# Kernel optimization log

Hardware: AMD Instinct MI355X
Metric: run time of the kernel (lower is better)

The kernel has to match this reference:

```python
import jax, jax.numpy as jnp
import numpy as np

DIM, H, DH = 3072, 24, 128
MLP = int(DIM * 4.0)
EPS = 1e-6


def setup_inputs() -> dict:
    key = jax.random.key(0)
    ks = jax.random.split(key, 8)
    B, L = 2, 4096
    s = 0.02
    return {
        "hidden_states": jax.random.normal(ks[0], (B, L, DIM), jnp.float32),
        "temb": jax.random.normal(ks[1], (B, DIM), jnp.float32),
        "rope": jax.random.normal(ks[2], (L, DH // 2, 4), jnp.float32),
        "w_lin": jax.random.normal(ks[3], (DIM, 3 * DIM), jnp.float32) * s,
        "b_lin": jnp.zeros((3 * DIM,), jnp.float32),
        "w1": jax.random.normal(ks[4], (DIM, 3 * DIM + MLP), jnp.float32) * s,
        "b1": jnp.zeros((3 * DIM + MLP,), jnp.float32),
        "w2": jax.random.normal(ks[5], (DIM + MLP, DIM), jnp.float32) * s,
        "b2": jnp.zeros((DIM,), jnp.float32),
        "q_scale": jnp.ones((DH,), jnp.float32),
        "k_scale": jnp.ones((DH,), jnp.float32),
    }


def _rms(x, scale):
    return x * jax.lax.rsqrt(jnp.mean(x * x, axis=-1, keepdims=True) + EPS) * scale


def _rope(x, fr):
    # x: [B,H,L,DH]; fr: [L, DH//2, 2, 2]
    B, Hn, L, D = x.shape
    x_ = x.reshape(B, Hn, L, D // 2, 1, 2)
    out = fr[..., 0] * x_[..., 0] + fr[..., 1] * x_[..., 1]  # [B,H,L,D//2,2]
    return out.reshape(B, Hn, L, D)


def reference(hidden_states, temb, rope, w_lin, b_lin, w1, b1, w2, b2, q_scale, k_scale):
    B, L, _ = hidden_states.shape
    residual = hidden_states
    # AdaLayerNormZeroSingle
    emb = jax.nn.silu(temb) @ w_lin + b_lin  # [B, 3*DIM]
    shift, scale, gate = jnp.split(emb[:, None, :], 3, axis=-1)
    mu = jnp.mean(hidden_states, axis=-1, keepdims=True)
    var = jnp.mean(jnp.square(hidden_states - mu), axis=-1, keepdims=True)
    x = (hidden_states - mu) * jax.lax.rsqrt(var + EPS)
    x = x * (1 + scale) + shift
    # fused QKV + MLP projection
    proj = x @ w1 + b1
    qkv, mlp = proj[..., : 3 * DIM], proj[..., 3 * DIM :]
    qkv = qkv.reshape(B, L, 3, H, DH).transpose(2, 0, 3, 1, 4)  # [3,B,H,L,DH]
    q, k, v = qkv[0], qkv[1], qkv[2]
    q = _rms(q, q_scale)
    k = _rms(k, k_scale)
    fr = rope.reshape(L, DH // 2, 2, 2)
    q = _rope(q, fr)
    k = _rope(k, fr)
    # heads are MERGED before attention (faithful to source)
    q = q.transpose(0, 2, 1, 3).reshape(B, L, H * DH)
    k = k.transpose(0, 2, 1, 3).reshape(B, L, H * DH)
    v = v.transpose(0, 2, 1, 3).reshape(B, L, H * DH)
    attn = jax.nn.softmax(jnp.einsum("bqd,bkd->bqk", q, k) * (DH ** -0.5), axis=-1)
    attn_out = jnp.einsum("bqk,bkd->bqd", attn, v)
    h = jnp.concatenate([attn_out, jax.nn.gelu(mlp)], axis=-1) @ w2 + b2
    return residual + gate * h
```

## Files before the change

kernel.cpp:

```cpp
#include <hip/hip_runtime.h>
#include <hip/hip_fp16.h>

typedef _Float16 half_t;
typedef __attribute__((ext_vector_type(8))) _Float16 f16x8;
typedef __attribute__((ext_vector_type(4))) float f32x4;

#define DIM   3072
#define NH    24
#define DH    128
#define MLP_D 12288
#define LSEQ  4096
#define BATCH 2
#define NROWS 8192
#define N1    21504
#define QKV_N 9216
#define CAT_N 15360

__device__ __forceinline__ void gload16(const void* g, void* l) {
  __builtin_amdgcn_global_load_lds((const __attribute__((address_space(1))) void*)g,
                                   (__attribute__((address_space(3))) void*)l, 16, 0, 0);
}

__device__ __forceinline__ float gelu_tanh(float x) {
  float u = 0.7978845608028654f * (x + 0.044715f * x * x * x);
  float t = 1.f - 2.f / (__expf(2.f * u) + 1.f);
  return 0.5f * x * (1.f + t);
}

struct EpiParams {
  const float* bias;
  float* outF; int ldoF;
  half_t* o1; int ldo1;
  half_t* o2; int ldo2;
  const float* resid;
  const float* gate;
  float scale;
};

template<int EPI>
__global__ __launch_bounds__(512, 2) void gemm256(
    const half_t* __restrict__ A, int lda,
    const half_t* __restrict__ B, int ldb,
    int nbx, int nby, int nsplit, int K, EpiParams ep)
{
  __shared__ __align__(16) char lds[131072];
  const int t = threadIdx.x, lane = t & 63, wid = t >> 6;

  const int nwg = nbx * nby;
  const int wg = blockIdx.x;
  const int id = (wg & 7) * (nwg >> 3) + (wg >> 3);
  const int panel = 8 * nbx;
  const int bm = (id / panel) * 8 + (id % 8);
  const int bn = (id % panel) / 8;
  const int brow = bm * 256, bcol = bn * 256;
  const int wr = wid >> 2, wc = wid & 3;

  f32x4 acc[8][4];
#pragma unroll
  for (int m = 0; m < 8; ++m)
#pragma unroll
    for (int n = 0; n < 4; ++n) acc[m][n] = (f32x4){0.f, 0.f, 0.f, 0.f};

  const int sperm = (((lane & 7) ^ (lane >> 3)) * 8);
  const half_t* pA = A + (size_t)(brow + wid * 32 + (lane >> 3)) * lda + sperm;
  const half_t* pB = B + (size_t)(bcol + wid * 32 + (lane >> 3)) * ldb + sperm;
  char* ldsA = lds + wid * 4096;
  const int NT = K >> 6;

#define STAGE(bufsel, tk)                                                  \
  {                                                                        \
    char* la = ldsA + (bufsel) * 65536;                                    \
    const half_t* ga = pA + (size_t)(tk) * 64;                             \
    const half_t* gb = pB + (size_t)(tk) * 64;                             \
    _Pragma("unroll")                                                      \
    for (int c = 0; c < 4; ++c) {                                          \
      gload16(ga + (size_t)c * 8 * lda, la + c * 1024);                    \
      gload16(gb + (size_t)c * 8 * ldb, la + 32768 + c * 1024);            \
    }                                                                      \
  }

  STAGE(0, 0);
  STAGE(1, 1);

  const int laneR = lane & 15;
  const int slot0 = (((lane >> 4) ^ (lane & 7)) << 4);
  const char* arow0 = lds + (size_t)(wr * 128 + laneR) * 128;
  const char* brow0 = lds + 32768 + (size_t)(wc * 64 + laneR) * 128;

  for (int tt = 0; tt < NT; ++tt) {
    const int cur = tt & 1;
    if (tt == NT - 1) asm volatile("s_waitcnt vmcnt(0)" ::: "memory");
    else              asm volatile("s_waitcnt vmcnt(8)" ::: "memory");
    __builtin_amdgcn_s_barrier();
    __builtin_amdgcn_sched_barrier(0);

    const char* ar = arow0 + cur * 65536;
    const char* br = brow0 + cur * 65536;
#pragma unroll
    for (int kk = 0; kk < 2; ++kk) {
      const int slot = slot0 ^ (kk << 6);
      f16x8 af[8], bf[4];
#pragma unroll
      for (int mi = 0; mi < 8; ++mi) af[mi] = *(const f16x8*)(ar + mi * 2048 + slot);
#pragma unroll
      for (int nj = 0; nj < 4; ++nj) bf[nj] = *(const f16x8*)(br + nj * 2048 + slot);
#pragma unroll
      for (int mi = 0; mi < 8; ++mi)
#pragma unroll
        for (int nj = 0; nj < 4; ++nj)
          acc[mi][nj] = __builtin_amdgcn_mfma_f32_16x16x32_f16(af[mi], bf[nj], acc[mi][nj], 0, 0, 0);
    }

    asm volatile("" ::: "memory");
    __builtin_amdgcn_sched_barrier(0);
    __builtin_amdgcn_s_barrier();
    if (tt + 2 < NT) STAGE(cur, tt + 2);
  }
#undef STAGE

  const int colb = bcol + wc * 64;
  const int rowb = brow + wr * 128 + (lane >> 4) * 4;
#pragma unroll
  for (int mi = 0; mi < 8; ++mi) {
#pragma unroll
    for (int nj = 0; nj < 4; ++nj) {
      int col = colb + nj * 16 + laneR;
#pragma unroll
      for (int j = 0; j < 4; ++j) {
        int row = rowb + mi * 16 + j;
        float v = acc[mi][nj][j];
        if (EPI == 0) {
          v += ep.bias[col];
          if (col < nsplit) {
            ep.o1[(size_t)row * ep.ldo1 + col] = (half_t)v;
          } else {
            ep.o2[(size_t)row * ep.ldo2 + DIM + (col - nsplit)] = (half_t)gelu_tanh(v);
          }
        } else if (EPI == 1) {
          ep.outF[(size_t)row * ep.ldoF + col] = v * ep.scale;
        } else if (EPI == 2) {
          ep.o2[(size_t)row * ep.ldo2 + col] = (half_t)v;
        } else {
          v += ep.bias[col];
          int b = row >> 12;
          float g = ep.gate[(size_t)b * QKV_N + col];
          float r = ep.resid[(size_t)row * DIM + col];
          ep.outF[(size_t)row * ep.ldoF + col] = r + g * v;
        }
      }
    }
  }
}

__global__ __launch_bounds__(256) void k_emb(
    const float* __restrict__ temb, const float* __restrict__ w_lin,
    const float* __restrict__ b_lin, float* __restrict__ emb)
{
  __shared__ float s[DIM];
  int b = blockIdx.y;
  int col = blockIdx.x * 256 + threadIdx.x;
  const float* tr = temb + (size_t)b * DIM;
  for (int k = threadIdx.x; k < DIM; k += 256) {
    float x = tr[k];
    s[k] = x / (1.f + __expf(-x));
  }
  __syncthreads();
  float acc = b_lin[col];
  for (int k = 0; k < DIM; k += 4) {
    acc += s[k] * w_lin[(size_t)k * QKV_N + col]
         + s[k + 1] * w_lin[(size_t)(k + 1) * QKV_N + col]
         + s[k + 2] * w_lin[(size_t)(k + 2) * QKV_N + col]
         + s[k + 3] * w_lin[(size_t)(k + 3) * QKV_N + col];
  }
  emb[(size_t)b * QKV_N + col] = acc;
}

__global__ __launch_bounds__(256) void k_lnmod(
    const float* __restrict__ hs, const float* __restrict__ emb,
    half_t* __restrict__ xmod)
{
  int row = blockIdx.x;
  int b = row >> 12;
  const float* x = hs + (size_t)row * DIM;
  int t = threadIdx.x;
  float s = 0.f, s2 = 0.f;
  float4 v[3];
#pragma unroll
  for (int i = 0; i < 3; ++i) {
    v[i] = ((const float4*)x)[t + 256 * i];
    s  += v[i].x + v[i].y + v[i].z + v[i].w;
    s2 += v[i].x * v[i].x + v[i].y * v[i].y + v[i].z * v[i].z + v[i].w * v[i].w;
  }
  for (int o = 32; o; o >>= 1) { s += __shfl_xor(s, o); s2 += __shfl_xor(s2, o); }
  __shared__ float rs[4], rs2[4];
  int lane = t & 63, w = t >> 6;
  if (lane == 0) { rs[w] = s; rs2[w] = s2; }
  __syncthreads();
  s = rs[0] + rs[1] + rs[2] + rs[3];
  s2 = rs2[0] + rs2[1] + rs2[2] + rs2[3];
  float mu = s * (1.f / DIM);
  float var = s2 * (1.f / DIM) - mu * mu;
  float rstd = rsqrtf(var + 1e-6f);
  const float* shift = emb + (size_t)b * QKV_N;
  const float* scale = shift + DIM;
#pragma unroll
  for (int i = 0; i < 3; ++i) {
    int g = t + 256 * i;
    float4 sc = ((const float4*)scale)[g];
    float4 sh = ((const float4*)shift)[g];
    half_t ob[4];
    float vv[4] = {v[i].x, v[i].y, v[i].z, v[i].w};
    float scv[4] = {sc.x, sc.y, sc.z, sc.w};
    float shv[4] = {sh.x, sh.y, sh.z, sh.w};
#pragma unroll
    for (int j = 0; j < 4; ++j) {
      float xn = (vv[j] - mu) * rstd;
      ob[j] = (half_t)(xn * (1.f + scv[j]) + shv[j]);
    }
    *(uint2*)&xmod[(size_t)row * DIM + g * 4] = *(uint2*)ob;
  }
}

__global__ __launch_bounds__(256) void k_transpose_cvt(
    const float* __restrict__ in, half_t* __restrict__ out, int R, int C)
{
  __shared__ float s[64][65];
  int c0 = blockIdx.x * 64, r0 = blockIdx.y * 64;
  int tx = threadIdx.x & 63, ty = threadIdx.x >> 6;
#pragma unroll
  for (int j = 0; j < 16; ++j) {
    int r = ty + j * 4;
    s[r][tx] = in[(size_t)(r0 + r) * C + c0 + tx];
  }
  __syncthreads();
#pragma unroll
  for (int j = 0; j < 16; ++j) {
    int c = ty + j * 4;
    out[(size_t)(c0 + c) * R + r0 + tx] = (half_t)s[tx][c];
  }
}

__global__ __launch_bounds__(256) void k_qk_rmsrope(
    half_t* __restrict__ qkv, const float* __restrict__ rope,
    const float* __restrict__ q_scale, const float* __restrict__ k_scale)
{
  int w = blockIdx.x * 4 + (threadIdx.x >> 6);
  int lane = threadIdx.x & 63;
  int qk = w & 1;
  int hr = w >> 1;
  int h = hr % 24;
  int bl = hr / 24;
  size_t base = (size_t)bl * QKV_N + qk * DIM + h * DH;
  float x0 = (float)qkv[base + lane * 2];
  float x1 = (float)qkv[base + lane * 2 + 1];
  float ss = x0 * x0 + x1 * x1;
  for (int o = 32; o; o >>= 1) ss += __shfl_xor(ss, o);
  float r = rsqrtf(ss * (1.f / DH) + 1e-6f);
  const float* sc = qk ? k_scale : q_scale;
  float xs0 = x0 * r * sc[lane * 2];
  float xs1 = x1 * r * sc[lane * 2 + 1];
  int l = bl & (LSEQ - 1);
  float4 fr = ((const float4*)rope)[(size_t)l * 64 + lane];
  qkv[base + lane * 2]     = (half_t)(fr.x * xs0 + fr.y * xs1);
  qkv[base + lane * 2 + 1] = (half_t)(fr.z * xs0 + fr.w * xs1);
}

__global__ __launch_bounds__(256) void k_vT(
    const half_t* __restrict__ qkv, half_t* __restrict__ vT)
{
  __shared__ half_t s[64][65];
  int b = blockIdx.z;
  int l0 = blockIdx.x * 64, d0 = blockIdx.y * 64;
  int tx = threadIdx.x & 63, ty = threadIdx.x >> 6;
#pragma unroll
  for (int j = 0; j < 16; ++j) {
    int l = ty + j * 4;
    s[l][tx] = qkv[(size_t)(b * LSEQ + l0 + l) * QKV_N + 2 * DIM + d0 + tx];
  }
  __syncthreads();
#pragma unroll
  for (int j = 0; j < 16; ++j) {
    int d = ty + j * 4;
    vT[((size_t)b * DIM + d0 + d) * LSEQ + l0 + tx] = s[tx][d];
  }
}

__global__ __launch_bounds__(256) void k_softmax(
    const float* __restrict__ S, half_t* __restrict__ P)
{
  int row = blockIdx.x;
  const float* srow = S + (size_t)row * LSEQ;
  int t = threadIdx.x;
  float4 v[4];
  float mx = -1e30f;
#pragma unroll
  for (int i = 0; i < 4; ++i) {
    v[i] = ((const float4*)srow)[t + 256 * i];
    mx = fmaxf(mx, fmaxf(fmaxf(v[i].x, v[i].y), fmaxf(v[i].z, v[i].w)));
  }
  for (int o = 32; o; o >>= 1) mx = fmaxf(mx, __shfl_xor(mx, o));
  __shared__ float rmx[4], rsum[4];
  int lane = t & 63, w = t >> 6;
  if (lane == 0) rmx[w] = mx;
  __syncthreads();
  mx = fmaxf(fmaxf(rmx[0], rmx[1]), fmaxf(rmx[2], rmx[3]));
  float s = 0.f;
#pragma unroll
  for (int i = 0; i < 4; ++i) {
    v[i].x = __expf(v[i].x - mx); v[i].y = __expf(v[i].y - mx);
    v[i].z = __expf(v[i].z - mx); v[i].w = __expf(v[i].w - mx);
    s += v[i].x + v[i].y + v[i].z + v[i].w;
  }
  for (int o = 32; o; o >>= 1) s += __shfl_xor(s, o);
  if (lane == 0) rsum[w] = s;
  __syncthreads();
  s = rsum[0] + rsum[1] + rsum[2] + rsum[3];
  float inv = 1.f / s;
#pragma unroll
  for (int i = 0; i < 4; ++i) {
    half_t ob[4] = {
      (half_t)(v[i].x * inv), (half_t)(v[i].y * inv),
      (half_t)(v[i].z * inv), (half_t)(v[i].w * inv)};
    *(uint2*)&P[(size_t)row * LSEQ + (t + 256 * i) * 4] = *(uint2*)ob;
  }
}

extern "C" void kernel_launch(void* const* d_in, const int* in_sizes, int n_in,
                              void* d_out, int out_size, void* d_ws, size_t ws_size,
                              hipStream_t stream) {
  const float* hs      = (const float*)d_in[0];
  const float* temb    = (const float*)d_in[1];
  const float* rope    = (const float*)d_in[2];
  const float* w_lin   = (const float*)d_in[3];
  const float* b_lin   = (const float*)d_in[4];
  const float* w1      = (const float*)d_in[5];
  const float* b1      = (const float*)d_in[6];
  const float* w2      = (const float*)d_in[7];
  const float* b2      = (const float*)d_in[8];
  const float* q_scale = (const float*)d_in[9];
  const float* k_scale = (const float*)d_in[10];
  float* out = (float*)d_out;

  char* ws = (char*)d_ws;
  size_t off = 0;
  auto alloc = [&](size_t bytes) { char* p = ws + off; off += (bytes + 255) & ~(size_t)255; return p; };
  float*  emb    = (float*) alloc((size_t)BATCH * QKV_N * 4);
  half_t* xmod   = (half_t*)alloc((size_t)NROWS * DIM * 2);
  half_t* w1T    = (half_t*)alloc((size_t)N1 * DIM * 2);
  half_t* w2T    = (half_t*)alloc((size_t)DIM * CAT_N * 2);
  half_t* qkv    = (half_t*)alloc((size_t)NROWS * QKV_N * 2);
  half_t* concat = (half_t*)alloc((size_t)NROWS * CAT_N * 2);
  half_t* vT     = (half_t*)alloc((size_t)BATCH * DIM * LSEQ * 2);
  float*  Sbuf   = (float*) alloc((size_t)LSEQ * LSEQ * 4);
  half_t* Pbuf   = (half_t*)alloc((size_t)LSEQ * LSEQ * 2);
  (void)ws_size; (void)n_in; (void)in_sizes; (void)out_size;

  k_emb<<<dim3(QKV_N / 256, BATCH), 256, 0, stream>>>(temb, w_lin, b_lin, emb);
  k_transpose_cvt<<<dim3(N1 / 64, DIM / 64), 256, 0, stream>>>(w1, w1T, DIM, N1);
  k_transpose_cvt<<<dim3(DIM / 64, CAT_N / 64), 256, 0, stream>>>(w2, w2T, CAT_N, DIM);
  k_lnmod<<<NROWS, 256, 0, stream>>>(hs, emb, xmod);

  EpiParams ep1 = {b1, nullptr, 0, qkv, QKV_N, concat, CAT_N, nullptr, nullptr, 0.f};
  gemm256<0><<<(N1 / 256) * (NROWS / 256), 512, 0, stream>>>(
      xmod, DIM, w1T, DIM, N1 / 256, NROWS / 256, QKV_N, DIM, ep1);

  k_qk_rmsrope<<<(NROWS * NH * 2) / 4, 256, 0, stream>>>(qkv, rope, q_scale, k_scale);
  k_vT<<<dim3(LSEQ / 64, DIM / 64, BATCH), 256, 0, stream>>>(qkv, vT);

  for (int b = 0; b < BATCH; ++b) {
    const half_t* qb = qkv + (size_t)b * LSEQ * QKV_N;
    EpiParams epS = {nullptr, Sbuf, LSEQ, nullptr, 0, nullptr, 0, nullptr, nullptr, 0.08838834764831845f};
    gemm256<1><<<(LSEQ / 256) * (LSEQ / 256), 512, 0, stream>>>(
        qb, QKV_N, qb + DIM, QKV_N, LSEQ / 256, LSEQ / 256, 0, DIM, epS);
    k_softmax<<<LSEQ, 256, 0, stream>>>(Sbuf, Pbuf);
    EpiParams epPV = {nullptr, nullptr, 0, nullptr, 0,
                      concat + (size_t)b * LSEQ * CAT_N, CAT_N, nullptr, nullptr, 0.f};
    gemm256<2><<<(DIM / 256) * (LSEQ / 256), 512, 0, stream>>>(
        Pbuf, LSEQ, vT + (size_t)b * DIM * LSEQ, LSEQ, DIM / 256, LSEQ / 256, 0, LSEQ, epPV);
  }

  EpiParams ep2 = {b2, out, DIM, nullptr, 0, nullptr, 0, hs, emb + 2 * DIM, 0.f};
  gemm256<3><<<(DIM / 256) * (NROWS / 256), 512, 0, stream>>>(
      concat, CAT_N, w2T, CAT_N, DIM / 256, NROWS / 256, 0, CAT_N, ep2);
}
```

Measured before the change: 3.053 ms.

## Split GEMM main loop into four interleaved phases with staggered async loads

```diff
diff --git a/kernel.cpp b/kernel.cpp
--- a/kernel.cpp
+++ b/kernel.cpp
@@ -61,63 +61,113 @@
 #pragma unroll
     for (int n = 0; n < 4; ++n) acc[m][n] = (f32x4){0.f, 0.f, 0.f, 0.f};
 
-  const int sperm = (((lane & 7) ^ (lane >> 3)) * 8);
-  const half_t* pA = A + (size_t)(brow + wid * 32 + (lane >> 3)) * lda + sperm;
-  const half_t* pB = B + (size_t)(bcol + wid * 32 + (lane >> 3)) * ldb + sperm;
-  char* ldsA = lds + wid * 4096;
+  const int scol = (((lane & 3) ^ ((lane >> 3) & 3)) * 8);
+  const half_t* pA = A + (size_t)(brow + wid * 32 + (lane >> 2)) * lda + scol;
+  const half_t* pB = B + (size_t)(bcol + wid * 32 + (lane >> 2)) * ldb + scol;
+  const int wrow = wid * 2048;
   const int NT = K >> 6;
 
-#define STAGE(bufsel, tk)                                                  \
-  {                                                                        \
-    char* la = ldsA + (bufsel) * 65536;                                    \
-    const half_t* ga = pA + (size_t)(tk) * 64;                             \
-    const half_t* gb = pB + (size_t)(tk) * 64;                             \
-    _Pragma("unroll")                                                      \
-    for (int c = 0; c < 4; ++c) {                                          \
-      gload16(ga + (size_t)c * 8 * lda, la + c * 1024);                    \
-      gload16(gb + (size_t)c * 8 * ldb, la + 32768 + c * 1024);            \
-    }                                                                      \
-  }
-
-  STAGE(0, 0);
-  STAGE(1, 1);
+  const int pc = (((lane >> 4) ^ ((lane >> 1) & 3)) << 4);
+  const int aoff = (wr * 128 + (lane & 15)) * 64 + pc;
+  const int boff = 32768 + (wc * 64 + (lane & 15)) * 64 + pc;
+
+  f16x8 bf[2][4];
+
+#define STAGE_A(bb, kh, tk) {                                               \
+    gload16(pA + (size_t)(tk) * 64 + (kh) * 32,                             \
+            (bb) + (kh) * 16384 + wrow);                                    \
+    gload16(pA + (size_t)(tk) * 64 + (kh) * 32 + (size_t)16 * lda,          \
+            (bb) + (kh) * 16384 + wrow + 1024); }
+#define STAGE_B(bb, kh, tk) {                                               \
+    gload16(pB + (size_t)(tk) * 64 + (kh) * 32,                             \
+            (bb) + 32768 + (kh) * 16384 + wrow);                            \
+    gload16(pB + (size_t)(tk) * 64 + (kh) * 32 + (size_t)16 * ldb,          \
+            (bb) + 32768 + (kh) * 16384 + wrow + 1024); }
+
+  {
+    char* b0 = lds;
+    char* b1 = lds + 65536;
+    STAGE_B(b0, 0, 0); STAGE_A(b0, 0, 0); STAGE_B(b0, 1, 0);
+    STAGE_A(b0, 1, 0); STAGE_B(b1, 0, 1); STAGE_A(b1, 0, 1); STAGE_B(b1, 1, 1);
+    asm volatile("s_waitcnt vmcnt(6)" ::: "memory");
+    __builtin_amdgcn_s_barrier();
+  }
+
+#define PHASE_TAIL                                                          \
+    __builtin_amdgcn_sched_barrier(0);                                      \
+    __builtin_amdgcn_s_barrier();                                           \
+    asm volatile("s_waitcnt lgkmcnt(0)" ::: "memory");                      \
+    __builtin_amdgcn_sched_barrier(0);                                      \
+    __builtin_amdgcn_s_setprio(1);
+
+#define PHASE_END                                                           \
+    __builtin_amdgcn_s_setprio(0);                                          \
+    __builtin_amdgcn_sched_barrier(0);                                      \
+    __builtin_amdgcn_s_barrier();
+
+  for (int tt = 0; tt < NT; ++tt) {
+    char* cb = lds + (size_t)(tt & 1) * 65536;
+    char* nb = lds + (size_t)((tt & 1) ^ 1) * 65536;
+    f16x8 af[4];
+
+#pragma unroll
+    for (int mi = 0; mi < 4; ++mi) af[mi] = *(const f16x8*)(cb + aoff + mi * 1024);
+#pragma unroll
+    for (int nj = 0; nj < 4; ++nj) bf[0][nj] = *(const f16x8*)(cb + boff + nj * 1024);
+    if (tt + 1 < NT) STAGE_A(nb, 1, tt + 1);
+    PHASE_TAIL
+#pragma unroll
+    for (int mi = 0; mi < 4; ++mi)
+#pragma unroll
+      for (int nj = 0; nj < 4; ++nj)
+        acc[mi][nj] = __builtin_amdgcn_mfma_f32_16x16x32_f16(af[mi], bf[0][nj], acc[mi][nj], 0, 0, 0);
+    PHASE_END
+
+#pragma unroll
+    for (int mi = 0; mi < 4; ++mi) af[mi] = *(const f16x8*)(cb + aoff + 4096 + mi * 1024);
+#pragma unroll
+    for (int nj = 0; nj < 4; ++nj) bf[1][nj] = *(const f16x8*)(cb + boff + 16384 + nj * 1024);
+    if (tt + 2 < NT) STAGE_B(cb, 0, tt + 2);
+    PHASE_TAIL
+#pragma unroll
+    for (int mi = 0; mi < 4; ++mi)
+#pragma unroll
+      for (int nj = 0; nj < 4; ++nj)
+        acc[4 + mi][nj] = __builtin_amdgcn_mfma_f32_16x16x32_f16(af[mi], bf[0][nj], acc[4 + mi][nj], 0, 0, 0);
+    PHASE_END
+
+#pragma unroll
+    for (int mi = 0; mi < 4; ++mi) af[mi] = *(const f16x8*)(cb + aoff + 16384 + mi * 1024);
+    if (tt + 2 < NT) STAGE_A(cb, 0, tt + 2);
+    PHASE_TAIL
+#pragma unroll
+    for (int mi = 0; mi < 4; ++mi)
+#pragma unroll
+      for (int nj = 0; nj < 4; ++nj)
+        acc[mi][nj] = __builtin_amdgcn_mfma_f32_16x16x32_f16(af[mi], bf[1][nj], acc[mi][nj], 0, 0, 0);
+    PHASE_END
+
+#pragma unroll
+    for (int mi = 0; mi < 4; ++mi) af[mi] = *(const f16x8*)(cb + aoff + 16384 + 4096 + mi * 1024);
+    if (tt + 2 < NT) STAGE_B(cb, 1, tt + 2);
+    PHASE_TAIL
+#pragma unroll
+    for (int mi = 0; mi < 4; ++mi)
+#pragma unroll
+      for (int nj = 0; nj < 4; ++nj)
+        acc[4 + mi][nj] = __builtin_amdgcn_mfma_f32_16x16x32_f16(af[mi], bf[1][nj], acc[4 + mi][nj], 0, 0, 0);
+    __builtin_amdgcn_s_setprio(0);
+    __builtin_amdgcn_sched_barrier(0);
+    if (tt + 2 < NT) asm volatile("s_waitcnt vmcnt(6)" ::: "memory");
+    else             asm volatile("s_waitcnt vmcnt(0)" ::: "memory");
+    __builtin_amdgcn_s_barrier();
+  }
+#undef STAGE_A
+#undef STAGE_B
+#undef PHASE_TAIL
+#undef PHASE_END
 
   const int laneR = lane & 15;
-  const int slot0 = (((lane >> 4) ^ (lane & 7)) << 4);
-  const char* arow0 = lds + (size_t)(wr * 128 + laneR) * 128;
-  const char* brow0 = lds + 32768 + (size_t)(wc * 64 + laneR) * 128;
-
-  for (int tt = 0; tt < NT; ++tt) {
-    const int cur = tt & 1;
-    if (tt == NT - 1) asm volatile("s_waitcnt vmcnt(0)" ::: "memory");
-    else              asm volatile("s_waitcnt vmcnt(8)" ::: "memory");
-    __builtin_amdgcn_s_barrier();
-    __builtin_amdgcn_sched_barrier(0);
-
-    const char* ar = arow0 + cur * 65536;
-    const char* br = brow0 + cur * 65536;
-#pragma unroll
-    for (int kk = 0; kk < 2; ++kk) {
-      const int slot = slot0 ^ (kk << 6);
-      f16x8 af[8], bf[4];
-#pragma unroll
-      for (int mi = 0; mi < 8; ++mi) af[mi] = *(const f16x8*)(ar + mi * 2048 + slot);
-#pragma unroll
-      for (int nj = 0; nj < 4; ++nj) bf[nj] = *(const f16x8*)(br + nj * 2048 + slot);
-#pragma unroll
-      for (int mi = 0; mi < 8; ++mi)
-#pragma unroll
-        for (int nj = 0; nj < 4; ++nj)
-          acc[mi][nj] = __builtin_amdgcn_mfma_f32_16x16x32_f16(af[mi], bf[nj], acc[mi][nj], 0, 0, 0);
-    }
-
-    asm volatile("" ::: "memory");
-    __builtin_amdgcn_sched_barrier(0);
-    __builtin_amdgcn_s_barrier();
-    if (tt + 2 < NT) STAGE(cur, tt + 2);
-  }
-#undef STAGE
-
   const int colb = bcol + wc * 64;
   const int rowb = brow + wr * 128 + (lane >> 4) * 4;
 #pragma unroll
```

New measurement: 2.930 ms. -4.0%, faster.

## Restructure GEMM main loop into 4-stage K=32 pipeline with register prefetch

Applied to the files above, without the earlier changes.

```diff
diff --git a/kernel.cpp b/kernel.cpp
--- a/kernel.cpp
+++ b/kernel.cpp
@@ -61,63 +61,87 @@
 #pragma unroll
     for (int n = 0; n < 4; ++n) acc[m][n] = (f32x4){0.f, 0.f, 0.f, 0.f};
 
-  const int sperm = (((lane & 7) ^ (lane >> 3)) * 8);
-  const half_t* pA = A + (size_t)(brow + wid * 32 + (lane >> 3)) * lda + sperm;
-  const half_t* pB = B + (size_t)(bcol + wid * 32 + (lane >> 3)) * ldb + sperm;
-  char* ldsA = lds + wid * 4096;
-  const int NT = K >> 6;
-
-#define STAGE(bufsel, tk)                                                  \
-  {                                                                        \
-    char* la = ldsA + (bufsel) * 65536;                                    \
-    const half_t* ga = pA + (size_t)(tk) * 64;                             \
-    const half_t* gb = pB + (size_t)(tk) * 64;                             \
-    _Pragma("unroll")                                                      \
-    for (int c = 0; c < 4; ++c) {                                          \
-      gload16(ga + (size_t)c * 8 * lda, la + c * 1024);                    \
-      gload16(gb + (size_t)c * 8 * ldb, la + 32768 + c * 1024);            \
-    }                                                                      \
-  }
-
-  STAGE(0, 0);
-  STAGE(1, 1);
+  const int scol = (((lane & 3) ^ ((lane >> 3) & 3)) * 8);
+  const half_t* pA = A + (size_t)(brow + wid * 32 + (lane >> 2)) * lda + scol;
+  const half_t* pB = B + (size_t)(bcol + wid * 32 + (lane >> 2)) * ldb + scol;
+  const int wrow = wid * 2048;
+  const int NT = K >> 5;
+
+  const int pc = (((lane >> 4) ^ ((lane >> 1) & 3)) << 4);
+  const int arow = (wr * 128 + (lane & 15)) * 64 + pc;
+  const int brow_o = 16384 + (wc * 64 + (lane & 15)) * 64 + pc;
+
+  f16x8 af[4], af2[4], bfA[4], bfB[4];
+
+#define STAGE(tk) {                                                         \
+    char* sb = lds + (((tk) & 3) << 15);                                    \
+    const half_t* ga = pA + (size_t)(tk) * 32;                              \
+    const half_t* gb = pB + (size_t)(tk) * 32;                              \
+    gload16(ga, sb + wrow);                                                 \
+    gload16(ga + (size_t)16 * lda, sb + wrow + 1024);                       \
+    gload16(gb, sb + 16384 + wrow);                                         \
+    gload16(gb + (size_t)16 * ldb, sb + 16384 + wrow + 1024); }
+
+#define MFMAC(base, AF, BF)                                                 \
+    __builtin_amdgcn_s_setprio(1);                                          \
+    _Pragma("unroll")                                                       \
+    for (int mi = 0; mi < 4; ++mi)                                          \
+      _Pragma("unroll")                                                     \
+      for (int nj = 0; nj < 4; ++nj)                                        \
+        acc[(base) + mi][nj] = __builtin_amdgcn_mfma_f32_16x16x32_f16(      \
+            AF[mi], BF[nj], acc[(base) + mi][nj], 0, 0, 0);                 \
+    __builtin_amdgcn_s_setprio(0);
+
+#define BODY(tt, BFC, BFN) {                                                \
+    char* cb = lds + (((tt) & 3) << 15);                                    \
+    af2[0] = *(const f16x8*)(cb + arow + 4096);                             \
+    af2[1] = *(const f16x8*)(cb + arow + 5120);                             \
+    af2[2] = *(const f16x8*)(cb + arow + 6144);                             \
+    af2[3] = *(const f16x8*)(cb + arow + 7168);                             \
+    MFMAC(0, af, BFC)                                                       \
+    if ((tt) + 3 < NT) STAGE((tt) + 3);                                     \
+    __builtin_amdgcn_sched_barrier(0);                                      \
+    if ((tt) + 3 < NT)      asm volatile("s_waitcnt vmcnt(8)" ::: "memory");\
+    else if ((tt) + 2 < NT) asm volatile("s_waitcnt vmcnt(4)" ::: "memory");\
+    else                    asm volatile("s_waitcnt vmcnt(0)" ::: "memory");\
+    __builtin_amdgcn_s_barrier();                                           \
+    __builtin_amdgcn_sched_barrier(0);                                      \
+    if ((tt) + 1 < NT) {                                                    \
+      char* fb = lds + ((((tt) + 1) & 3) << 15);                            \
+      af[0] = *(const f16x8*)(fb + arow);                                   \
+      af[1] = *(const f16x8*)(fb + arow + 1024);                            \
+      af[2] = *(const f16x8*)(fb + arow + 2048);                            \
+      af[3] = *(const f16x8*)(fb + arow + 3072);                            \
+      BFN[0] = *(const f16x8*)(fb + brow_o);                                \
+      BFN[1] = *(const f16x8*)(fb + brow_o + 1024);                         \
+      BFN[2] = *(const f16x8*)(fb + brow_o + 2048);                         \
+      BFN[3] = *(const f16x8*)(fb + brow_o + 3072);                         \
+    }                                                                       \
+    MFMAC(4, af2, BFC)                                                      \
+  }
+
+  STAGE(0); STAGE(1); STAGE(2);
+  asm volatile("s_waitcnt vmcnt(8)" ::: "memory");
+  __builtin_amdgcn_s_barrier();
+  __builtin_amdgcn_sched_barrier(0);
+  af[0] = *(const f16x8*)(lds + arow);
+  af[1] = *(const f16x8*)(lds + arow + 1024);
+  af[2] = *(const f16x8*)(lds + arow + 2048);
+  af[3] = *(const f16x8*)(lds + arow + 3072);
+  bfA[0] = *(const f16x8*)(lds + brow_o);
+  bfA[1] = *(const f16x8*)(lds + brow_o + 1024);
+  bfA[2] = *(const f16x8*)(lds + brow_o + 2048);
+  bfA[3] = *(const f16x8*)(lds + brow_o + 3072);
+
+  for (int tt = 0; tt < NT; tt += 2) {
+    BODY(tt, bfA, bfB)
+    BODY(tt + 1, bfB, bfA)
+  }
+#undef STAGE
+#undef MFMAC
+#undef BODY
 
   const int laneR = lane & 15;
-  const int slot0 = (((lane >> 4) ^ (lane & 7)) << 4);
-  const char* arow0 = lds + (size_t)(wr * 128 + laneR) * 128;
-  const char* brow0 = lds + 32768 + (size_t)(wc * 64 + laneR) * 128;
-
-  for (int tt = 0; tt < NT; ++tt) {
-    const int cur = tt & 1;
-    if (tt == NT - 1) asm volatile("s_waitcnt vmcnt(0)" ::: "memory");
-    else              asm volatile("s_waitcnt vmcnt(8)" ::: "memory");
-    __builtin_amdgcn_s_barrier();
-    __builtin_amdgcn_sched_barrier(0);
-
-    const char* ar = arow0 + cur * 65536;
-    const char* br = brow0 + cur * 65536;
-#pragma unroll
-    for (int kk = 0; kk < 2; ++kk) {
-      const int slot = slot0 ^ (kk << 6);
-      f16x8 af[8], bf[4];
-#pragma unroll
-      for (int mi = 0; mi < 8; ++mi) af[mi] = *(const f16x8*)(ar + mi * 2048 + slot);
-#pragma unroll
-      for (int nj = 0; nj < 4; ++nj) bf[nj] = *(const f16x8*)(br + nj * 2048 + slot);
-#pragma unroll
-      for (int mi = 0; mi < 8; ++mi)
-#pragma unroll
-        for (int nj = 0; nj < 4; ++nj)
-          acc[mi][nj] = __builtin_amdgcn_mfma_f32_16x16x32_f16(af[mi], bf[nj], acc[mi][nj], 0, 0, 0);
-    }
-
-    asm volatile("" ::: "memory");
-    __builtin_amdgcn_sched_barrier(0);
-    __builtin_amdgcn_s_barrier();
-    if (tt + 2 < NT) STAGE(cur, tt + 2);
-  }
-#undef STAGE
-
   const int colb = bcol + wc * 64;
   const int rowb = brow + wr * 128 + (lane >> 4) * 4;
 #pragma unroll
```

New measurement: 2.858 ms. 6.4% less time.

## Restructure GEMM mainloop into 4-stage BK=32 pipeline with split phases

Applied to the files above, without the earlier changes.

```diff
diff --git a/kernel.cpp b/kernel.cpp
--- a/kernel.cpp
+++ b/kernel.cpp
@@ -61,63 +61,87 @@
 #pragma unroll
     for (int n = 0; n < 4; ++n) acc[m][n] = (f32x4){0.f, 0.f, 0.f, 0.f};
 
-  const int sperm = (((lane & 7) ^ (lane >> 3)) * 8);
-  const half_t* pA = A + (size_t)(brow + wid * 32 + (lane >> 3)) * lda + sperm;
-  const half_t* pB = B + (size_t)(bcol + wid * 32 + (lane >> 3)) * ldb + sperm;
-  char* ldsA = lds + wid * 4096;
-  const int NT = K >> 6;
-
-#define STAGE(bufsel, tk)                                                  \
-  {                                                                        \
-    char* la = ldsA + (bufsel) * 65536;                                    \
-    const half_t* ga = pA + (size_t)(tk) * 64;                             \
-    const half_t* gb = pB + (size_t)(tk) * 64;                             \
-    _Pragma("unroll")                                                      \
-    for (int c = 0; c < 4; ++c) {                                          \
-      gload16(ga + (size_t)c * 8 * lda, la + c * 1024);                    \
-      gload16(gb + (size_t)c * 8 * ldb, la + 32768 + c * 1024);            \
-    }                                                                      \
-  }
-
-  STAGE(0, 0);
-  STAGE(1, 1);
+  const int scol = (((lane & 3) ^ ((lane >> 3) & 3)) * 8);
+  const half_t* pA = A + (size_t)(brow + wid * 32 + (lane >> 2)) * lda + scol;
+  const half_t* pB = B + (size_t)(bcol + wid * 32 + (lane >> 2)) * ldb + scol;
+  const int wrow = wid * 2048;
+  const int NT = K >> 5;
+
+  const int pc = (((lane >> 4) ^ ((lane >> 1) & 3)) << 4);
+  const int arow = (wr * 128 + (lane & 15)) * 64 + pc;
+  const int brow_o = 16384 + (wc * 64 + (lane & 15)) * 64 + pc;
+
+  f16x8 af[4], af2[4], bfA[4];
+
+#define STAGE_A(tk) {                                                       \
+    char* sb = lds + (((tk) & 3) << 15);                                    \
+    const half_t* ga = pA + (size_t)(tk) * 32;                              \
+    gload16(ga, sb + wrow);                                                 \
+    gload16(ga + (size_t)16 * lda, sb + wrow + 1024); }
+#define STAGE_B(tk) {                                                       \
+    char* sb = lds + (((tk) & 3) << 15);                                    \
+    const half_t* gb = pB + (size_t)(tk) * 32;                              \
+    gload16(gb, sb + 16384 + wrow);                                         \
+    gload16(gb + (size_t)16 * ldb, sb + 16384 + wrow + 1024); }
+
+  STAGE_A(0) STAGE_B(0) STAGE_A(1) STAGE_B(1) STAGE_A(2) STAGE_B(2)
+  asm volatile("s_waitcnt vmcnt(8)" ::: "memory");
+  __builtin_amdgcn_s_barrier();
+
+  for (int tt = 0; tt < NT; ++tt) {
+    char* cb = lds + (size_t)((tt & 3) << 15);
+
+    af[0]  = *(const f16x8*)(cb + arow);
+    af[1]  = *(const f16x8*)(cb + arow + 1024);
+    af[2]  = *(const f16x8*)(cb + arow + 2048);
+    af[3]  = *(const f16x8*)(cb + arow + 3072);
+    bfA[0] = *(const f16x8*)(cb + brow_o);
+    bfA[1] = *(const f16x8*)(cb + brow_o + 1024);
+    bfA[2] = *(const f16x8*)(cb + brow_o + 2048);
+    bfA[3] = *(const f16x8*)(cb + brow_o + 3072);
+    if (tt + 3 < NT) STAGE_A(tt + 3)
+    __builtin_amdgcn_sched_barrier(0);
+    __builtin_amdgcn_s_barrier();
+    asm volatile("s_waitcnt lgkmcnt(0)" ::: "memory");
+    __builtin_amdgcn_sched_barrier(0);
+    __builtin_amdgcn_s_setprio(1);
+#pragma unroll
+    for (int mi = 0; mi < 4; ++mi)
+#pragma unroll
+      for (int nj = 0; nj < 4; ++nj)
+        acc[mi][nj] = __builtin_amdgcn_mfma_f32_16x16x32_f16(
+            af[mi], bfA[nj], acc[mi][nj], 0, 0, 0);
+    __builtin_amdgcn_s_setprio(0);
+    __builtin_amdgcn_sched_barrier(0);
+    __builtin_amdgcn_s_barrier();
+
+    af2[0] = *(const f16x8*)(cb + arow + 4096);
+    af2[1] = *(const f16x8*)(cb + arow + 5120);
+    af2[2] = *(const f16x8*)(cb + arow + 6144);
+    af2[3] = *(const f16x8*)(cb + arow + 7168);
+    if (tt + 3 < NT) STAGE_B(tt + 3)
+    __builtin_amdgcn_sched_barrier(0);
+    __builtin_amdgcn_s_barrier();
+    asm volatile("s_waitcnt lgkmcnt(0)" ::: "memory");
+    __builtin_amdgcn_sched_barrier(0);
+    __builtin_amdgcn_s_setprio(1);
+#pragma unroll
+    for (int mi = 0; mi < 4; ++mi)
+#pragma unroll
+      for (int nj = 0; nj < 4; ++nj)
+        acc[4 + mi][nj] = __builtin_amdgcn_mfma_f32_16x16x32_f16(
+            af2[mi], bfA[nj], acc[4 + mi][nj], 0, 0, 0);
+    __builtin_amdgcn_s_setprio(0);
+    __builtin_amdgcn_sched_barrier(0);
+    if (tt + 3 < NT)      asm volatile("s_waitcnt vmcnt(8)" ::: "memory");
+    else if (tt + 2 < NT) asm volatile("s_waitcnt vmcnt(4)" ::: "memory");
+    else if (tt + 1 < NT) asm volatile("s_waitcnt vmcnt(0)" ::: "memory");
+    __builtin_amdgcn_s_barrier();
+  }
+#undef STAGE_A
+#undef STAGE_B
 
   const int laneR = lane & 15;
-  const int slot0 = (((lane >> 4) ^ (lane & 7)) << 4);
-  const char* arow0 = lds + (size_t)(wr * 128 + laneR) * 128;
-  const char* brow0 = lds + 32768 + (size_t)(wc * 64 + laneR) * 128;
-
-  for (int tt = 0; tt < NT; ++tt) {
-    const int cur = tt & 1;
-    if (tt == NT - 1) asm volatile("s_waitcnt vmcnt(0)" ::: "memory");
-    else              asm volatile("s_waitcnt vmcnt(8)" ::: "memory");
-    __builtin_amdgcn_s_barrier();
-    __builtin_amdgcn_sched_barrier(0);
-
-    const char* ar = arow0 + cur * 65536;
-    const char* br = brow0 + cur * 65536;
-#pragma unroll
-    for (int kk = 0; kk < 2; ++kk) {
-      const int slot = slot0 ^ (kk << 6);
-      f16x8 af[8], bf[4];
-#pragma unroll
-      for (int mi = 0; mi < 8; ++mi) af[mi] = *(const f16x8*)(ar + mi * 2048 + slot);
-#pragma unroll
-      for (int nj = 0; nj < 4; ++nj) bf[nj] = *(const f16x8*)(br + nj * 2048 + slot);
-#pragma unroll
-      for (int mi = 0; mi < 8; ++mi)
-#pragma unroll
-        for (int nj = 0; nj < 4; ++nj)
-          acc[mi][nj] = __builtin_amdgcn_mfma_f32_16x16x32_f16(af[mi], bf[nj], acc[mi][nj], 0, 0, 0);
-    }
-
-    asm volatile("" ::: "memory");
-    __builtin_amdgcn_sched_barrier(0);
-    __builtin_amdgcn_s_barrier();
-    if (tt + 2 < NT) STAGE(cur, tt + 2);
-  }
-#undef STAGE
-
   const int colb = bcol + wc * 64;
   const int rowb = brow + wr * 128 + (lane >> 4) * 4;
 #pragma unroll
```

Result: faster. 2.965 ms (-2.9%).
